# Kernel optimization log

Hardware: AMD Instinct MI355X
Metric: run time of the kernel (lower is better)

The kernel has to match this reference:

```python
import jax, jax.numpy as jnp
import numpy as np

E = 64        # num_local_experts
N = 32768     # total permuted tokens
H = 1024      # hidden_dim
F = 1024      # intermediate_dim
C = N // E    # per-expert capacity (setup uses equal token counts)


def setup_inputs() -> dict:
    key = jax.random.key(0)
    k1, k2, k3, k4 = jax.random.split(key, 4)
    s = 0.02  # init scale
    return {
        "permuted_local_hidden_states": jax.random.normal(k1, (N, H), jnp.float32),
        "tokens_per_expert": jnp.full((E,), C, dtype=jnp.int32),
        "w_gate": jax.random.normal(k2, (E, H, F), jnp.float32) * s,
        "w_up": jax.random.normal(k3, (E, H, F), jnp.float32) * s,
        "w_down": jax.random.normal(k4, (E, F, H), jnp.float32) * s,
    }


def reference(permuted_local_hidden_states, tokens_per_expert, w_gate, w_up, w_down):
    x = permuted_local_hidden_states  # [N, H], sorted by expert
    counts = tokens_per_expert.astype(jnp.int32)  # [E]
    # start offset of each expert's contiguous token range (torch cumsum + cat([0]))
    starts = jnp.concatenate([jnp.zeros((1,), jnp.int32), jnp.cumsum(counts)])[:-1]
    # expert id and within-expert position for every token (jit-friendly dispatch)
    eid = jnp.repeat(jnp.arange(E, dtype=jnp.int32), counts, total_repeat_length=N)
    pos = jnp.arange(N, dtype=jnp.int32) - starts[eid]
    # gather tokens into fixed-capacity per-expert buffer [E, C, H]; unused slots stay 0
    buf = jnp.zeros((E, C, H), x.dtype).at[eid, pos].set(x)
    # grouped LLaMA MLP: down( silu(gate(x)) * up(x) ), one GEMM triple per expert, batched
    gate = jnp.einsum('ech,ehf->ecf', buf, w_gate)
    up = jnp.einsum('ech,ehf->ecf', buf, w_up)
    h = jax.nn.silu(gate) * up                      # [E, C, F]
    out_buf = jnp.einsum('ecf,efh->ech', h, w_down)  # [E, C, H]
    # scatter back to flat token order (output_local[start:end] = output)
    output_local = out_buf[eid, pos]  # [N, H]
    return output_local
```

## Files before the change

kernel.cpp:

```cpp
#include <hip/hip_runtime.h>
#include <stdint.h>


#define NUM_E 64
#define DIM_H 1024
#define DIM_F 1024
#define CAP   512
#define NTOK  32768

typedef short short8 __attribute__((ext_vector_type(8)));
typedef float f32x4 __attribute__((ext_vector_type(4)));

#define VMCNT(n)  asm volatile("s_waitcnt vmcnt(" #n ")" ::: "memory")
#define LGKMCNT0  asm volatile("s_waitcnt lgkmcnt(0)" ::: "memory")
#define SBAR      __builtin_amdgcn_s_barrier()
#define SCHED0    __builtin_amdgcn_sched_barrier(0)

__device__ __forceinline__ uint32_t cvtpk(float lo, float hi) {
  uint32_t r;
  asm("v_cvt_pk_bf16_f32 %0, %1, %2" : "=v"(r) : "v"(lo), "v"(hi));
  return r;
}
__device__ __forceinline__ unsigned short f2bf(float a) {
  uint32_t ua = __builtin_bit_cast(uint32_t, a);
  ua += 0x7FFFu + ((ua >> 16) & 1u);
  return (unsigned short)(ua >> 16);
}
__device__ __forceinline__ void gload_lds16(const void* g, void* l) {
  __builtin_amdgcn_global_load_lds((const __attribute__((address_space(1))) uint32_t*)g,
                                   (__attribute__((address_space(3))) uint32_t*)l, 16, 0, 0);
}

__global__ __launch_bounds__(256) void cvt_kernel(const float* __restrict__ x,
                                                  unsigned short* __restrict__ xbf) {
  size_t i = ((size_t)blockIdx.x * 256 + threadIdx.x) * 8;
  f32x4 a = *reinterpret_cast<const f32x4*>(x + i);
  f32x4 b = *reinterpret_cast<const f32x4*>(x + i + 4);
  int4 o = make_int4((int)cvtpk(a[0], a[1]), (int)cvtpk(a[2], a[3]),
                     (int)cvtpk(b[0], b[1]), (int)cvtpk(b[2], b[3]));
  *reinterpret_cast<int4*>(xbf + i) = o;
}

__global__ __launch_bounds__(512, 2) void gateup_kernel_v3(
    const unsigned short* __restrict__ xbf, const float* __restrict__ wg,
    const float* __restrict__ wu, unsigned short* __restrict__ hout)
{
  __shared__ unsigned char smem[131072];
  const int t = threadIdx.x;
  int bid = blockIdx.x;
  bid = (bid & 7) * 128 + (bid >> 3);
  const int e = bid >> 4, rr = bid & 15, mb = rr >> 3, nb = rr & 7;
  const int row0 = e * CAP + mb * 256;
  const int col0 = nb * 128;
  const unsigned short* Ag = xbf + (size_t)row0 * DIM_H;
  const float* Bgg = wg + (size_t)e * (DIM_H * DIM_F) + col0;
  const float* Bug = wu + (size_t)e * (DIM_H * DIM_F) + col0;

  const int lane = t & 63, wid = t >> 6;
  const int wm = wid >> 1, wn = wid & 1;

  f32x4 accg[4][4], accu[4][4];
  #pragma unroll
  for (int i = 0; i < 4; i++)
    #pragma unroll
    for (int j = 0; j < 4; j++) {
      accg[i][j] = f32x4{0.f, 0.f, 0.f, 0.f};
      accu[i][j] = f32x4{0.f, 0.f, 0.f, 0.f};
    }

  const int bn = t & 127, bkb = (t >> 7) * 16;
  float bg[16], bu[16];

  auto loadB = [&](int k0) {
    #pragma unroll
    for (int i = 0; i < 16; i++) {
      bg[i] = Bgg[(size_t)(k0 + bkb + i) * DIM_F + bn];
      bu[i] = Bug[(size_t)(k0 + bkb + i) * DIM_F + bn];
    }
  };
  auto writeB = [&](int b) {
    const int Bb = 65536 + b * 32768;
    #pragma unroll
    for (int j = 0; j < 4; j++) {
      int off = Bb + bn * 128 + (((bkb + j * 4) * 2) ^ ((bn & 7) << 4));
      *reinterpret_cast<uint2*>(&smem[off]) =
          make_uint2(cvtpk(bg[j*4+0], bg[j*4+1]), cvtpk(bg[j*4+2], bg[j*4+3]));
      *reinterpret_cast<uint2*>(&smem[off + 16384]) =
          make_uint2(cvtpk(bu[j*4+0], bu[j*4+1]), cvtpk(bu[j*4+2], bu[j*4+3]));
    }
  };
  auto loadA = [&](int k0, int buf) {
    #pragma unroll
    for (int j = 0; j < 4; j++) {
      int lin = (j * 512 + t) * 16;
      int r = lin >> 7;
      int q = (lin >> 4) & 7;
      const void* src = (const unsigned char*)Ag + (size_t)r * 2048 + k0 * 2 + ((q ^ (r & 7)) * 16);
      gload_lds16(src, &smem[buf * 32768 + lin]);
    }
  };
  auto compute = [&](int kt) {
    const int Ab = (kt & 1) * 32768;
    const int Bb = 65536 + (kt & 1) * 32768;
    __builtin_amdgcn_s_setprio(1);
    #pragma unroll
    for (int kk = 0; kk < 2; kk++) {
      short8 a[4], bgf[4], buf_[4];
      #pragma unroll
      for (int mi = 0; mi < 4; mi++) {
        int r = wm * 64 + mi * 16 + (lane & 15);
        a[mi] = *reinterpret_cast<const short8*>(
            &smem[Ab + r * 128 + ((kk * 64 + (lane >> 4) * 16) ^ ((r & 7) << 4))]);
      }
      #pragma unroll
      for (int ni = 0; ni < 4; ni++) {
        int n = wn * 64 + ni * 16 + (lane & 15);
        int off = Bb + n * 128 + ((kk * 64 + (lane >> 4) * 16) ^ ((n & 7) << 4));
        bgf[ni]  = *reinterpret_cast<const short8*>(&smem[off]);
        buf_[ni] = *reinterpret_cast<const short8*>(&smem[off + 16384]);
      }
      #pragma unroll
      for (int mi = 0; mi < 4; mi++)
        #pragma unroll
        for (int ni = 0; ni < 4; ni++) {
          accg[mi][ni] = __builtin_amdgcn_mfma_f32_16x16x32_bf16(a[mi], bgf[ni],  accg[mi][ni], 0, 0, 0);
          accu[mi][ni] = __builtin_amdgcn_mfma_f32_16x16x32_bf16(a[mi], buf_[ni], accu[mi][ni], 0, 0, 0);
        }
    }
    __builtin_amdgcn_s_setprio(0);
  };

  const int NT = DIM_H / 64;
  loadB(0);
  loadA(0, 0);
  VMCNT(4); SCHED0;
  writeB(0);
  LGKMCNT0; VMCNT(0); SCHED0;
  SBAR;
  for (int kt = 0; kt < NT; kt++) {
    if (kt + 1 < NT) {
      loadB((kt + 1) * 64);
      loadA((kt + 1) * 64, (kt + 1) & 1);
      SCHED0;
    }
    compute(kt);
    if (kt + 1 < NT) {
      VMCNT(4); SCHED0;
      writeB((kt + 1) & 1);
      LGKMCNT0; VMCNT(0); SCHED0;
      SBAR;
    }
  }

  #pragma unroll
  for (int mi = 0; mi < 4; mi++)
    #pragma unroll
    for (int ni = 0; ni < 4; ni++) {
      int col = col0 + wn * 64 + ni * 16 + (lane & 15);
      int rbase = row0 + wm * 64 + mi * 16 + (lane >> 4) * 4;
      #pragma unroll
      for (int j = 0; j < 4; j++) {
        float g = accg[mi][ni][j], u = accu[mi][ni][j];
        float hv = (g / (1.f + __expf(-g))) * u;
        hout[(size_t)(rbase + j) * DIM_F + col] = f2bf(hv);
      }
    }
}

__global__ __launch_bounds__(512, 2) void down_kernel_v3(
    const unsigned short* __restrict__ hin, const float* __restrict__ wd,
    float* __restrict__ out)
{
  __shared__ unsigned char smem[98304];
  const int t = threadIdx.x;
  int bid = blockIdx.x;
  bid = (bid & 7) * 128 + (bid >> 3);
  const int e = bid >> 4, rr = bid & 15, mb = rr >> 3, nb = rr & 7;
  const int row0 = e * CAP + mb * 256;
  const int col0 = nb * 128;
  const unsigned short* Ag = hin + (size_t)row0 * DIM_F;
  const float* Bdg = wd + (size_t)e * (DIM_F * DIM_H) + col0;

  const int lane = t & 63, wid = t >> 6;
  const int wm = wid >> 1, wn = wid & 1;

  f32x4 acc[4][4];
  #pragma unroll
  for (int i = 0; i < 4; i++)
    #pragma unroll
    for (int j = 0; j < 4; j++) acc[i][j] = f32x4{0.f, 0.f, 0.f, 0.f};

  const int bn = t & 127, bkb = (t >> 7) * 16;
  float bs[16];

  auto loadB = [&](int k0) {
    #pragma unroll
    for (int i = 0; i < 16; i++)
      bs[i] = Bdg[(size_t)(k0 + bkb + i) * DIM_H + bn];
  };
  auto writeB = [&](int b) {
    const int Bb = 65536 + b * 16384;
    #pragma unroll
    for (int j = 0; j < 4; j++) {
      int off = Bb + bn * 128 + (((bkb + j * 4) * 2) ^ ((bn & 7) << 4));
      *reinterpret_cast<uint2*>(&smem[off]) =
          make_uint2(cvtpk(bs[j*4+0], bs[j*4+1]), cvtpk(bs[j*4+2], bs[j*4+3]));
    }
  };
  auto loadA = [&](int k0, int buf) {
    #pragma unroll
    for (int j = 0; j < 4; j++) {
      int lin = (j * 512 + t) * 16;
      int r = lin >> 7;
      int q = (lin >> 4) & 7;
      const void* src = (const unsigned char*)Ag + (size_t)r * 2048 + k0 * 2 + ((q ^ (r & 7)) * 16);
      gload_lds16(src, &smem[buf * 32768 + lin]);
    }
  };
  auto compute = [&](int kt) {
    const int Ab = (kt & 1) * 32768;
    const int Bb = 65536 + (kt & 1) * 16384;
    __builtin_amdgcn_s_setprio(1);
    #pragma unroll
    for (int kk = 0; kk < 2; kk++) {
      short8 a[4], b[4];
      #pragma unroll
      for (int mi = 0; mi < 4; mi++) {
        int r = wm * 64 + mi * 16 + (lane & 15);
        a[mi] = *reinterpret_cast<const short8*>(
            &smem[Ab + r * 128 + ((kk * 64 + (lane >> 4) * 16) ^ ((r & 7) << 4))]);
      }
      #pragma unroll
      for (int ni = 0; ni < 4; ni++) {
        int n = wn * 64 + ni * 16 + (lane & 15);
        b[ni] = *reinterpret_cast<const short8*>(
            &smem[Bb + n * 128 + ((kk * 64 + (lane >> 4) * 16) ^ ((n & 7) << 4))]);
      }
      #pragma unroll
      for (int mi = 0; mi < 4; mi++)
        #pragma unroll
        for (int ni = 0; ni < 4; ni++)
          acc[mi][ni] = __builtin_amdgcn_mfma_f32_16x16x32_bf16(a[mi], b[ni], acc[mi][ni], 0, 0, 0);
    }
    __builtin_amdgcn_s_setprio(0);
  };

  const int NT = DIM_F / 64;
  loadB(0);
  loadA(0, 0);
  VMCNT(4); SCHED0;
  writeB(0);
  LGKMCNT0; VMCNT(0); SCHED0;
  SBAR;
  for (int kt = 0; kt < NT; kt++) {
    if (kt + 1 < NT) {
      loadB((kt + 1) * 64);
      loadA((kt + 1) * 64, (kt + 1) & 1);
      SCHED0;
    }
    compute(kt);
    if (kt + 1 < NT) {
      VMCNT(4); SCHED0;
      writeB((kt + 1) & 1);
      LGKMCNT0; VMCNT(0); SCHED0;
      SBAR;
    }
  }

  #pragma unroll
  for (int mi = 0; mi < 4; mi++)
    #pragma unroll
    for (int ni = 0; ni < 4; ni++) {
      int col = col0 + wn * 64 + ni * 16 + (lane & 15);
      int rbase = row0 + wm * 64 + mi * 16 + (lane >> 4) * 4;
      #pragma unroll
      for (int j = 0; j < 4; j++)
        out[(size_t)(rbase + j) * DIM_H + col] = acc[mi][ni][j];
    }
}

extern "C" void kernel_launch(void* const* d_in, const int* in_sizes, int n_in,
                              void* d_out, int out_size, void* d_ws, size_t ws_size,
                              hipStream_t stream) {
  (void)in_sizes; (void)n_in; (void)out_size; (void)ws_size;
  const float* x  = (const float*)d_in[0];
  const float* wg = (const float*)d_in[2];
  const float* wu = (const float*)d_in[3];
  const float* wd = (const float*)d_in[4];
  unsigned short* h   = (unsigned short*)d_ws;
  unsigned short* xbf = (unsigned short*)((char*)d_ws + (size_t)NTOK * DIM_F * 2);
  float* out = (float*)d_out;

  cvt_kernel<<<dim3((NTOK * DIM_H) / (256 * 8)), dim3(256), 0, stream>>>(x, xbf);
  gateup_kernel_v3<<<dim3(1024), dim3(512), 0, stream>>>(xbf, wg, wu, h);
  down_kernel_v3<<<dim3(1024), dim3(512), 0, stream>>>(h, wd, out);
}
```

Baseline: 365.2 us.

## Triple-buffer A tiles in LDS to prefetch two k-steps ahead

Both GEMM kernels now keep three LDS buffers for the A tile and issue the direct-to-LDS A load two iterations ahead instead of one. The waits move to vmcnt(4), so the newest A loads stay in flight across the barrier. This is meant to hide global-load latency for the activation operand behind compute. The cost is more LDS (160KB for gate/up, 128KB for down) and slightly more complex wait logic at the loop tail.

```diff
diff --git a/kernel.cpp b/kernel.cpp
--- a/kernel.cpp
+++ b/kernel.cpp
@@ -41,11 +41,11 @@
   *reinterpret_cast<int4*>(xbf + i) = o;
 }
 
-__global__ __launch_bounds__(512, 2) void gateup_kernel_v3(
+__global__ __launch_bounds__(512, 2) void gateup_kernel_v9(
     const unsigned short* __restrict__ xbf, const float* __restrict__ wg,
     const float* __restrict__ wu, unsigned short* __restrict__ hout)
 {
-  __shared__ unsigned char smem[131072];
+  __shared__ unsigned char smem[163840];
   const int t = threadIdx.x;
   int bid = blockIdx.x;
   bid = (bid & 7) * 128 + (bid >> 3);
@@ -79,7 +79,7 @@
     }
   };
   auto writeB = [&](int b) {
-    const int Bb = 65536 + b * 32768;
+    const int Bb = 98304 + b * 32768;
     #pragma unroll
     for (int j = 0; j < 4; j++) {
       int off = Bb + bn * 128 + (((bkb + j * 4) * 2) ^ ((bn & 7) << 4));
@@ -100,8 +100,8 @@
     }
   };
   auto compute = [&](int kt) {
-    const int Ab = (kt & 1) * 32768;
-    const int Bb = 65536 + (kt & 1) * 32768;
+    const int Ab = (kt % 3) * 32768;
+    const int Bb = 98304 + (kt & 1) * 32768;
     __builtin_amdgcn_s_setprio(1);
     #pragma unroll
     for (int kk = 0; kk < 2; kk++) {
@@ -133,21 +133,25 @@
   const int NT = DIM_H / 64;
   loadB(0);
   loadA(0, 0);
+  SCHED0;
   VMCNT(4); SCHED0;
   writeB(0);
-  LGKMCNT0; VMCNT(0); SCHED0;
+  loadA(64, 1);
+  SCHED0;
+  LGKMCNT0; VMCNT(4); SCHED0;
   SBAR;
   for (int kt = 0; kt < NT; kt++) {
     if (kt + 1 < NT) {
       loadB((kt + 1) * 64);
-      loadA((kt + 1) * 64, (kt + 1) & 1);
+      if (kt + 2 < NT) loadA((kt + 2) * 64, (kt + 2) % 3);
       SCHED0;
     }
     compute(kt);
     if (kt + 1 < NT) {
-      VMCNT(4); SCHED0;
+      if (kt + 2 < NT) { VMCNT(4); } else { VMCNT(0); }
+      SCHED0;
       writeB((kt + 1) & 1);
-      LGKMCNT0; VMCNT(0); SCHED0;
+      LGKMCNT0; SCHED0;
       SBAR;
     }
   }
@@ -160,18 +164,18 @@
       int rbase = row0 + wm * 64 + mi * 16 + (lane >> 4) * 4;
       #pragma unroll
       for (int j = 0; j < 4; j++) {
-        float g = accg[mi][ni][j], u = accu[mi][ni][j];
-        float hv = (g / (1.f + __expf(-g))) * u;
+        float gv = accg[mi][ni][j], uv = accu[mi][ni][j];
+        float hv = (gv / (1.f + __expf(-gv))) * uv;
         hout[(size_t)(rbase + j) * DIM_F + col] = f2bf(hv);
       }
     }
 }
 
-__global__ __launch_bounds__(512, 2) void down_kernel_v3(
+__global__ __launch_bounds__(512, 2) void down_kernel_v9(
     const unsigned short* __restrict__ hin, const float* __restrict__ wd,
     float* __restrict__ out)
 {
-  __shared__ unsigned char smem[98304];
+  __shared__ unsigned char smem[131072];
   const int t = threadIdx.x;
   int bid = blockIdx.x;
   bid = (bid & 7) * 128 + (bid >> 3);
@@ -199,7 +203,7 @@
       bs[i] = Bdg[(size_t)(k0 + bkb + i) * DIM_H + bn];
   };
   auto writeB = [&](int b) {
-    const int Bb = 65536 + b * 16384;
+    const int Bb = 98304 + b * 16384;
     #pragma unroll
     for (int j = 0; j < 4; j++) {
       int off = Bb + bn * 128 + (((bkb + j * 4) * 2) ^ ((bn & 7) << 4));
@@ -218,8 +222,8 @@
     }
   };
   auto compute = [&](int kt) {
-    const int Ab = (kt & 1) * 32768;
-    const int Bb = 65536 + (kt & 1) * 16384;
+    const int Ab = (kt % 3) * 32768;
+    const int Bb = 98304 + (kt & 1) * 16384;
     __builtin_amdgcn_s_setprio(1);
     #pragma unroll
     for (int kk = 0; kk < 2; kk++) {
@@ -248,21 +252,25 @@
   const int NT = DIM_F / 64;
   loadB(0);
   loadA(0, 0);
+  SCHED0;
   VMCNT(4); SCHED0;
   writeB(0);
-  LGKMCNT0; VMCNT(0); SCHED0;
+  loadA(64, 1);
+  SCHED0;
+  LGKMCNT0; VMCNT(4); SCHED0;
   SBAR;
   for (int kt = 0; kt < NT; kt++) {
     if (kt + 1 < NT) {
       loadB((kt + 1) * 64);
-      loadA((kt + 1) * 64, (kt + 1) & 1);
+      if (kt + 2 < NT) loadA((kt + 2) * 64, (kt + 2) % 3);
       SCHED0;
     }
     compute(kt);
     if (kt + 1 < NT) {
-      VMCNT(4); SCHED0;
+      if (kt + 2 < NT) { VMCNT(4); } else { VMCNT(0); }
+      SCHED0;
       writeB((kt + 1) & 1);
-      LGKMCNT0; VMCNT(0); SCHED0;
+      LGKMCNT0; SCHED0;
       SBAR;
     }
   }
@@ -292,6 +300,6 @@
   float* out = (float*)d_out;
 
   cvt_kernel<<<dim3((NTOK * DIM_H) / (256 * 8)), dim3(256), 0, stream>>>(x, xbf);
-  gateup_kernel_v3<<<dim3(1024), dim3(512), 0, stream>>>(xbf, wg, wu, h);
-  down_kernel_v3<<<dim3(1024), dim3(512), 0, stream>>>(h, wd, out);
-}
+  gateup_kernel_v9<<<dim3(1024), dim3(512), 0, stream>>>(xbf, wg, wu, h);
+  down_kernel_v9<<<dim3(1024), dim3(512), 0, stream>>>(h, wd, out);
+}
```

Result: no change. 369.5 us (+1.2%).

## Interleave LDS reads, global prefetch and MFMA clusters in four-phase K loop

Applied to the files above, without the earlier changes.

Both GEMM kernels restructure the per-K-tile loop into four barrier-separated phases. Each phase issues LDS fragment reads and a slice of the next tile's global loads (A, B first half, B second half, then the B write to LDS), followed by a prioritized MFMA cluster. The goal is to spread memory traffic across the compute phases and keep the matrix units fed, instead of one bulk load and write per tile. In exchange it adds many extra workgroup barriers per tile and uses #pragma unroll 1, which may add synchronization overhead.

```diff
diff --git a/kernel.cpp b/kernel.cpp
--- a/kernel.cpp
+++ b/kernel.cpp
@@ -15,6 +15,8 @@
 #define LGKMCNT0  asm volatile("s_waitcnt lgkmcnt(0)" ::: "memory")
 #define SBAR      __builtin_amdgcn_s_barrier()
 #define SCHED0    __builtin_amdgcn_sched_barrier(0)
+#define SP1       __builtin_amdgcn_s_setprio(1)
+#define SP0       __builtin_amdgcn_s_setprio(0)
 
 __device__ __forceinline__ uint32_t cvtpk(float lo, float hi) {
   uint32_t r;
@@ -41,7 +43,7 @@
   *reinterpret_cast<int4*>(xbf + i) = o;
 }
 
-__global__ __launch_bounds__(512, 2) void gateup_kernel_v3(
+__global__ __launch_bounds__(512, 2) void gateup_kernel_v11(
     const unsigned short* __restrict__ xbf, const float* __restrict__ wg,
     const float* __restrict__ wu, unsigned short* __restrict__ hout)
 {
@@ -71,9 +73,16 @@
   const int bn = t & 127, bkb = (t >> 7) * 16;
   float bg[16], bu[16];
 
-  auto loadB = [&](int k0) {
-    #pragma unroll
-    for (int i = 0; i < 16; i++) {
+  auto loadB1 = [&](int k0) {
+    #pragma unroll
+    for (int i = 0; i < 8; i++) {
+      bg[i] = Bgg[(size_t)(k0 + bkb + i) * DIM_F + bn];
+      bu[i] = Bug[(size_t)(k0 + bkb + i) * DIM_F + bn];
+    }
+  };
+  auto loadB2 = [&](int k0) {
+    #pragma unroll
+    for (int i = 8; i < 16; i++) {
       bg[i] = Bgg[(size_t)(k0 + bkb + i) * DIM_F + bn];
       bu[i] = Bug[(size_t)(k0 + bkb + i) * DIM_F + bn];
     }
@@ -99,57 +108,78 @@
       gload_lds16(src, &smem[buf * 32768 + lin]);
     }
   };
-  auto compute = [&](int kt) {
+  auto ldA = [&](short8 (&a)[4], int Ab, int kk) {
+    #pragma unroll
+    for (int mi = 0; mi < 4; mi++) {
+      int r = wm * 64 + mi * 16 + (lane & 15);
+      a[mi] = *reinterpret_cast<const short8*>(
+          &smem[Ab + r * 128 + ((kk * 64 + (lane >> 4) * 16) ^ ((r & 7) << 4))]);
+    }
+  };
+  auto ldB = [&](short8 (&bf)[4], int Bb, int kk, int uoff) {
+    #pragma unroll
+    for (int ni = 0; ni < 4; ni++) {
+      int n = wn * 64 + ni * 16 + (lane & 15);
+      bf[ni] = *reinterpret_cast<const short8*>(
+          &smem[Bb + uoff + n * 128 + ((kk * 64 + (lane >> 4) * 16) ^ ((n & 7) << 4))]);
+    }
+  };
+  auto mfq = [&](f32x4 (&acc)[4][4], const short8 (&a)[4], const short8 (&bf)[4]) {
+    SP1;
+    #pragma unroll
+    for (int mi = 0; mi < 4; mi++)
+      #pragma unroll
+      for (int ni = 0; ni < 4; ni++)
+        acc[mi][ni] = __builtin_amdgcn_mfma_f32_16x16x32_bf16(a[mi], bf[ni], acc[mi][ni], 0, 0, 0);
+    SP0;
+  };
+
+  const int NT = DIM_H / 64;
+  loadB1(0); loadB2(0);
+  loadA(0, 0);
+  SCHED0;
+  VMCNT(4); SCHED0;
+  writeB(0);
+  VMCNT(0); LGKMCNT0; SCHED0;
+  SBAR;
+
+  #pragma unroll 1
+  for (int kt = 0; kt < NT; kt++) {
     const int Ab = (kt & 1) * 32768;
     const int Bb = 65536 + (kt & 1) * 32768;
-    __builtin_amdgcn_s_setprio(1);
-    #pragma unroll
-    for (int kk = 0; kk < 2; kk++) {
-      short8 a[4], bgf[4], buf_[4];
-      #pragma unroll
-      for (int mi = 0; mi < 4; mi++) {
-        int r = wm * 64 + mi * 16 + (lane & 15);
-        a[mi] = *reinterpret_cast<const short8*>(
-            &smem[Ab + r * 128 + ((kk * 64 + (lane >> 4) * 16) ^ ((r & 7) << 4))]);
-      }
-      #pragma unroll
-      for (int ni = 0; ni < 4; ni++) {
-        int n = wn * 64 + ni * 16 + (lane & 15);
-        int off = Bb + n * 128 + ((kk * 64 + (lane >> 4) * 16) ^ ((n & 7) << 4));
-        bgf[ni]  = *reinterpret_cast<const short8*>(&smem[off]);
-        buf_[ni] = *reinterpret_cast<const short8*>(&smem[off + 16384]);
-      }
-      #pragma unroll
-      for (int mi = 0; mi < 4; mi++)
-        #pragma unroll
-        for (int ni = 0; ni < 4; ni++) {
-          accg[mi][ni] = __builtin_amdgcn_mfma_f32_16x16x32_bf16(a[mi], bgf[ni],  accg[mi][ni], 0, 0, 0);
-          accu[mi][ni] = __builtin_amdgcn_mfma_f32_16x16x32_bf16(a[mi], buf_[ni], accu[mi][ni], 0, 0, 0);
-        }
-    }
-    __builtin_amdgcn_s_setprio(0);
-  };
-
-  const int NT = DIM_H / 64;
-  loadB(0);
-  loadA(0, 0);
-  VMCNT(4); SCHED0;
-  writeB(0);
-  LGKMCNT0; VMCNT(0); SCHED0;
-  SBAR;
-  for (int kt = 0; kt < NT; kt++) {
-    if (kt + 1 < NT) {
-      loadB((kt + 1) * 64);
-      loadA((kt + 1) * 64, (kt + 1) & 1);
-      SCHED0;
-    }
-    compute(kt);
-    if (kt + 1 < NT) {
-      VMCNT(4); SCHED0;
+    const bool more = (kt + 1 < NT);
+    short8 a[4], bf[4];
+    ldA(a, Ab, 0); ldB(bf, Bb, 0, 0);
+    if (more) loadA((kt + 1) * 64, (kt + 1) & 1);
+    SCHED0;
+    SBAR;
+    LGKMCNT0; SCHED0;
+    mfq(accg, a, bf);
+    SBAR;
+    ldB(bf, Bb, 0, 16384);
+    if (more) loadB1((kt + 1) * 64);
+    SCHED0;
+    SBAR;
+    LGKMCNT0; SCHED0;
+    mfq(accu, a, bf);
+    SBAR;
+    ldA(a, Ab, 1); ldB(bf, Bb, 1, 0);
+    if (more) loadB2((kt + 1) * 64);
+    SCHED0;
+    SBAR;
+    LGKMCNT0; SCHED0;
+    mfq(accg, a, bf);
+    SBAR;
+    ldB(bf, Bb, 1, 16384);
+    if (more) {
+      VMCNT(0); SCHED0;
       writeB((kt + 1) & 1);
-      LGKMCNT0; VMCNT(0); SCHED0;
-      SBAR;
-    }
+    }
+    SCHED0;
+    SBAR;
+    LGKMCNT0; SCHED0;
+    mfq(accu, a, bf);
+    SBAR;
   }
 
   #pragma unroll
@@ -160,14 +190,14 @@
       int rbase = row0 + wm * 64 + mi * 16 + (lane >> 4) * 4;
       #pragma unroll
       for (int j = 0; j < 4; j++) {
-        float g = accg[mi][ni][j], u = accu[mi][ni][j];
-        float hv = (g / (1.f + __expf(-g))) * u;
+        float gv = accg[mi][ni][j], uv = accu[mi][ni][j];
+        float hv = (gv / (1.f + __expf(-gv))) * uv;
         hout[(size_t)(rbase + j) * DIM_F + col] = f2bf(hv);
       }
     }
 }
 
-__global__ __launch_bounds__(512, 2) void down_kernel_v3(
+__global__ __launch_bounds__(512, 2) void down_kernel_v11(
     const unsigned short* __restrict__ hin, const float* __restrict__ wd,
     float* __restrict__ out)
 {
@@ -193,9 +223,14 @@
   const int bn = t & 127, bkb = (t >> 7) * 16;
   float bs[16];
 
-  auto loadB = [&](int k0) {
-    #pragma unroll
-    for (int i = 0; i < 16; i++)
+  auto loadB1 = [&](int k0) {
+    #pragma unroll
+    for (int i = 0; i < 8; i++)
+      bs[i] = Bdg[(size_t)(k0 + bkb + i) * DIM_H + bn];
+  };
+  auto loadB2 = [&](int k0) {
+    #pragma unroll
+    for (int i = 8; i < 16; i++)
       bs[i] = Bdg[(size_t)(k0 + bkb + i) * DIM_H + bn];
   };
   auto writeB = [&](int b) {
@@ -217,54 +252,79 @@
       gload_lds16(src, &smem[buf * 32768 + lin]);
     }
   };
-  auto compute = [&](int kt) {
+  auto ldA = [&](short8 (&a)[4], int Ab, int kk) {
+    #pragma unroll
+    for (int mi = 0; mi < 4; mi++) {
+      int r = wm * 64 + mi * 16 + (lane & 15);
+      a[mi] = *reinterpret_cast<const short8*>(
+          &smem[Ab + r * 128 + ((kk * 64 + (lane >> 4) * 16) ^ ((r & 7) << 4))]);
+    }
+  };
+  auto ldB2f = [&](short8 (&bf)[2], int Bb, int kk, int nh) {
+    #pragma unroll
+    for (int i = 0; i < 2; i++) {
+      int n = wn * 64 + (nh * 2 + i) * 16 + (lane & 15);
+      bf[i] = *reinterpret_cast<const short8*>(
+          &smem[Bb + n * 128 + ((kk * 64 + (lane >> 4) * 16) ^ ((n & 7) << 4))]);
+    }
+  };
+  auto mf8 = [&](const short8 (&a)[4], const short8 (&bf)[2], int nh) {
+    SP1;
+    #pragma unroll
+    for (int mi = 0; mi < 4; mi++)
+      #pragma unroll
+      for (int i = 0; i < 2; i++)
+        acc[mi][nh * 2 + i] =
+            __builtin_amdgcn_mfma_f32_16x16x32_bf16(a[mi], bf[i], acc[mi][nh * 2 + i], 0, 0, 0);
+    SP0;
+  };
+
+  const int NT = DIM_F / 64;
+  loadB1(0); loadB2(0);
+  loadA(0, 0);
+  SCHED0;
+  VMCNT(4); SCHED0;
+  writeB(0);
+  VMCNT(0); LGKMCNT0; SCHED0;
+  SBAR;
+
+  #pragma unroll 1
+  for (int kt = 0; kt < NT; kt++) {
     const int Ab = (kt & 1) * 32768;
     const int Bb = 65536 + (kt & 1) * 16384;
-    __builtin_amdgcn_s_setprio(1);
-    #pragma unroll
-    for (int kk = 0; kk < 2; kk++) {
-      short8 a[4], b[4];
-      #pragma unroll
-      for (int mi = 0; mi < 4; mi++) {
-        int r = wm * 64 + mi * 16 + (lane & 15);
-        a[mi] = *reinterpret_cast<const short8*>(
-            &smem[Ab + r * 128 + ((kk * 64 + (lane >> 4) * 16) ^ ((r & 7) << 4))]);
-      }
-      #pragma unroll
-      for (int ni = 0; ni < 4; ni++) {
-        int n = wn * 64 + ni * 16 + (lane & 15);
-        b[ni] = *reinterpret_cast<const short8*>(
-            &smem[Bb + n * 128 + ((kk * 64 + (lane >> 4) * 16) ^ ((n & 7) << 4))]);
-      }
-      #pragma unroll
-      for (int mi = 0; mi < 4; mi++)
-        #pragma unroll
-        for (int ni = 0; ni < 4; ni++)
-          acc[mi][ni] = __builtin_amdgcn_mfma_f32_16x16x32_bf16(a[mi], b[ni], acc[mi][ni], 0, 0, 0);
-    }
-    __builtin_amdgcn_s_setprio(0);
-  };
-
-  const int NT = DIM_F / 64;
-  loadB(0);
-  loadA(0, 0);
-  VMCNT(4); SCHED0;
-  writeB(0);
-  LGKMCNT0; VMCNT(0); SCHED0;
-  SBAR;
-  for (int kt = 0; kt < NT; kt++) {
-    if (kt + 1 < NT) {
-      loadB((kt + 1) * 64);
-      loadA((kt + 1) * 64, (kt + 1) & 1);
-      SCHED0;
-    }
-    compute(kt);
-    if (kt + 1 < NT) {
-      VMCNT(4); SCHED0;
+    const bool more = (kt + 1 < NT);
+    short8 a[4], bf[2];
+    ldA(a, Ab, 0); ldB2f(bf, Bb, 0, 0);
+    if (more) loadA((kt + 1) * 64, (kt + 1) & 1);
+    SCHED0;
+    SBAR;
+    LGKMCNT0; SCHED0;
+    mf8(a, bf, 0);
+    SBAR;
+    ldB2f(bf, Bb, 0, 1);
+    if (more) loadB1((kt + 1) * 64);
+    SCHED0;
+    SBAR;
+    LGKMCNT0; SCHED0;
+    mf8(a, bf, 1);
+    SBAR;
+    ldA(a, Ab, 1); ldB2f(bf, Bb, 1, 0);
+    if (more) loadB2((kt + 1) * 64);
+    SCHED0;
+    SBAR;
+    LGKMCNT0; SCHED0;
+    mf8(a, bf, 0);
+    SBAR;
+    ldB2f(bf, Bb, 1, 1);
+    if (more) {
+      VMCNT(0); SCHED0;
       writeB((kt + 1) & 1);
-      LGKMCNT0; VMCNT(0); SCHED0;
-      SBAR;
-    }
+    }
+    SCHED0;
+    SBAR;
+    LGKMCNT0; SCHED0;
+    mf8(a, bf, 1);
+    SBAR;
   }
 
   #pragma unroll
@@ -292,6 +352,6 @@
   float* out = (float*)d_out;
 
   cvt_kernel<<<dim3((NTOK * DIM_H) / (256 * 8)), dim3(256), 0, stream>>>(x, xbf);
-  gateup_kernel_v3<<<dim3(1024), dim3(512), 0, stream>>>(xbf, wg, wu, h);
-  down_kernel_v3<<<dim3(1024), dim3(512), 0, stream>>>(h, wd, out);
-}
+  gateup_kernel_v11<<<dim3(1024), dim3(512), 0, stream>>>(xbf, wg, wu, h);
+  down_kernel_v11<<<dim3(1024), dim3(512), 0, stream>>>(h, wd, out);
+}
```

Result: slower. 442.7 us (+21.2%).

## Halve N tile to 64 and single-buffer B in LDS for higher occupancy

Applied to the files above, without the earlier changes.

Both GEMM kernels shrink the output tile from 256x128 to 256x64, doubling the grid to 2048 blocks and halving the accumulator registers. B in LDS goes from double-buffered to single-buffered, guarded by an extra barrier before each write, and each thread now writes B with one 16-byte store per matrix. LDS per block drops to 80KB and 72KB, and launch bounds now request four waves per SIMD, aiming to hide latency through more resident work. The cost is that each A tile is reloaded by twice as many blocks, arithmetic intensity per block falls, and the extra barrier per k-step can stall the pipeline.

```diff
diff --git a/kernel.cpp b/kernel.cpp
--- a/kernel.cpp
+++ b/kernel.cpp
@@ -41,17 +41,17 @@
   *reinterpret_cast<int4*>(xbf + i) = o;
 }
 
-__global__ __launch_bounds__(512, 2) void gateup_kernel_v3(
+__global__ __launch_bounds__(512, 4) void gateup_kernel_v12(
     const unsigned short* __restrict__ xbf, const float* __restrict__ wg,
     const float* __restrict__ wu, unsigned short* __restrict__ hout)
 {
-  __shared__ unsigned char smem[131072];
+  __shared__ unsigned char smem[81920];
   const int t = threadIdx.x;
   int bid = blockIdx.x;
-  bid = (bid & 7) * 128 + (bid >> 3);
-  const int e = bid >> 4, rr = bid & 15, mb = rr >> 3, nb = rr & 7;
+  bid = (bid & 7) * 256 + (bid >> 3);
+  const int e = bid >> 5, rr = bid & 31, mb = rr >> 4, nb = rr & 15;
   const int row0 = e * CAP + mb * 256;
-  const int col0 = nb * 128;
+  const int col0 = nb * 64;
   const unsigned short* Ag = xbf + (size_t)row0 * DIM_H;
   const float* Bgg = wg + (size_t)e * (DIM_H * DIM_F) + col0;
   const float* Bug = wu + (size_t)e * (DIM_H * DIM_F) + col0;
@@ -59,35 +59,33 @@
   const int lane = t & 63, wid = t >> 6;
   const int wm = wid >> 1, wn = wid & 1;
 
-  f32x4 accg[4][4], accu[4][4];
+  f32x4 accg[4][2], accu[4][2];
   #pragma unroll
   for (int i = 0; i < 4; i++)
     #pragma unroll
-    for (int j = 0; j < 4; j++) {
+    for (int j = 0; j < 2; j++) {
       accg[i][j] = f32x4{0.f, 0.f, 0.f, 0.f};
       accu[i][j] = f32x4{0.f, 0.f, 0.f, 0.f};
     }
 
-  const int bn = t & 127, bkb = (t >> 7) * 16;
-  float bg[16], bu[16];
+  const int bn = t & 63, bkb = (t >> 6) * 8;
+  float bg[8], bu[8];
 
   auto loadB = [&](int k0) {
     #pragma unroll
-    for (int i = 0; i < 16; i++) {
+    for (int i = 0; i < 8; i++) {
       bg[i] = Bgg[(size_t)(k0 + bkb + i) * DIM_F + bn];
       bu[i] = Bug[(size_t)(k0 + bkb + i) * DIM_F + bn];
     }
   };
-  auto writeB = [&](int b) {
-    const int Bb = 65536 + b * 32768;
-    #pragma unroll
-    for (int j = 0; j < 4; j++) {
-      int off = Bb + bn * 128 + (((bkb + j * 4) * 2) ^ ((bn & 7) << 4));
-      *reinterpret_cast<uint2*>(&smem[off]) =
-          make_uint2(cvtpk(bg[j*4+0], bg[j*4+1]), cvtpk(bg[j*4+2], bg[j*4+3]));
-      *reinterpret_cast<uint2*>(&smem[off + 16384]) =
-          make_uint2(cvtpk(bu[j*4+0], bu[j*4+1]), cvtpk(bu[j*4+2], bu[j*4+3]));
-    }
+  auto writeB = [&]() {
+    int off = 65536 + bn * 128 + ((bkb * 2) ^ ((bn & 7) << 4));
+    *reinterpret_cast<int4*>(&smem[off]) =
+        make_int4((int)cvtpk(bg[0], bg[1]), (int)cvtpk(bg[2], bg[3]),
+                  (int)cvtpk(bg[4], bg[5]), (int)cvtpk(bg[6], bg[7]));
+    *reinterpret_cast<int4*>(&smem[off + 8192]) =
+        make_int4((int)cvtpk(bu[0], bu[1]), (int)cvtpk(bu[2], bu[3]),
+                  (int)cvtpk(bu[4], bu[5]), (int)cvtpk(bu[6], bu[7]));
   };
   auto loadA = [&](int k0, int buf) {
     #pragma unroll
@@ -101,11 +99,10 @@
   };
   auto compute = [&](int kt) {
     const int Ab = (kt & 1) * 32768;
-    const int Bb = 65536 + (kt & 1) * 32768;
     __builtin_amdgcn_s_setprio(1);
     #pragma unroll
     for (int kk = 0; kk < 2; kk++) {
-      short8 a[4], bgf[4], buf_[4];
+      short8 a[4], bgf[2], buf_[2];
       #pragma unroll
       for (int mi = 0; mi < 4; mi++) {
         int r = wm * 64 + mi * 16 + (lane & 15);
@@ -113,16 +110,16 @@
             &smem[Ab + r * 128 + ((kk * 64 + (lane >> 4) * 16) ^ ((r & 7) << 4))]);
       }
       #pragma unroll
-      for (int ni = 0; ni < 4; ni++) {
-        int n = wn * 64 + ni * 16 + (lane & 15);
-        int off = Bb + n * 128 + ((kk * 64 + (lane >> 4) * 16) ^ ((n & 7) << 4));
+      for (int ni = 0; ni < 2; ni++) {
+        int n = wn * 32 + ni * 16 + (lane & 15);
+        int off = 65536 + n * 128 + ((kk * 64 + (lane >> 4) * 16) ^ ((n & 7) << 4));
         bgf[ni]  = *reinterpret_cast<const short8*>(&smem[off]);
-        buf_[ni] = *reinterpret_cast<const short8*>(&smem[off + 16384]);
+        buf_[ni] = *reinterpret_cast<const short8*>(&smem[off + 8192]);
       }
       #pragma unroll
       for (int mi = 0; mi < 4; mi++)
         #pragma unroll
-        for (int ni = 0; ni < 4; ni++) {
+        for (int ni = 0; ni < 2; ni++) {
           accg[mi][ni] = __builtin_amdgcn_mfma_f32_16x16x32_bf16(a[mi], bgf[ni],  accg[mi][ni], 0, 0, 0);
           accu[mi][ni] = __builtin_amdgcn_mfma_f32_16x16x32_bf16(a[mi], buf_[ni], accu[mi][ni], 0, 0, 0);
         }
@@ -133,21 +130,25 @@
   const int NT = DIM_H / 64;
   loadB(0);
   loadA(0, 0);
+  SCHED0;
   VMCNT(4); SCHED0;
-  writeB(0);
-  LGKMCNT0; VMCNT(0); SCHED0;
+  writeB();
+  VMCNT(0); LGKMCNT0; SCHED0;
   SBAR;
+  #pragma unroll 1
   for (int kt = 0; kt < NT; kt++) {
-    if (kt + 1 < NT) {
+    const bool more = (kt + 1 < NT);
+    if (more) {
       loadB((kt + 1) * 64);
       loadA((kt + 1) * 64, (kt + 1) & 1);
       SCHED0;
     }
     compute(kt);
-    if (kt + 1 < NT) {
+    if (more) {
+      SBAR;
       VMCNT(4); SCHED0;
-      writeB((kt + 1) & 1);
-      LGKMCNT0; VMCNT(0); SCHED0;
+      writeB();
+      VMCNT(0); LGKMCNT0; SCHED0;
       SBAR;
     }
   }
@@ -155,57 +156,54 @@
   #pragma unroll
   for (int mi = 0; mi < 4; mi++)
     #pragma unroll
-    for (int ni = 0; ni < 4; ni++) {
-      int col = col0 + wn * 64 + ni * 16 + (lane & 15);
+    for (int ni = 0; ni < 2; ni++) {
+      int col = col0 + wn * 32 + ni * 16 + (lane & 15);
       int rbase = row0 + wm * 64 + mi * 16 + (lane >> 4) * 4;
       #pragma unroll
       for (int j = 0; j < 4; j++) {
-        float g = accg[mi][ni][j], u = accu[mi][ni][j];
-        float hv = (g / (1.f + __expf(-g))) * u;
+        float gv = accg[mi][ni][j], uv = accu[mi][ni][j];
+        float hv = (gv / (1.f + __expf(-gv))) * uv;
         hout[(size_t)(rbase + j) * DIM_F + col] = f2bf(hv);
       }
     }
 }
 
-__global__ __launch_bounds__(512, 2) void down_kernel_v3(
+__global__ __launch_bounds__(512, 4) void down_kernel_v12(
     const unsigned short* __restrict__ hin, const float* __restrict__ wd,
     float* __restrict__ out)
 {
-  __shared__ unsigned char smem[98304];
+  __shared__ unsigned char smem[73728];
   const int t = threadIdx.x;
   int bid = blockIdx.x;
-  bid = (bid & 7) * 128 + (bid >> 3);
-  const int e = bid >> 4, rr = bid & 15, mb = rr >> 3, nb = rr & 7;
+  bid = (bid & 7) * 256 + (bid >> 3);
+  const int e = bid >> 5, rr = bid & 31, mb = rr >> 4, nb = rr & 15;
   const int row0 = e * CAP + mb * 256;
-  const int col0 = nb * 128;
+  const int col0 = nb * 64;
   const unsigned short* Ag = hin + (size_t)row0 * DIM_F;
   const float* Bdg = wd + (size_t)e * (DIM_F * DIM_H) + col0;
 
   const int lane = t & 63, wid = t >> 6;
   const int wm = wid >> 1, wn = wid & 1;
 
-  f32x4 acc[4][4];
+  f32x4 acc[4][2];
   #pragma unroll
   for (int i = 0; i < 4; i++)
     #pragma unroll
-    for (int j = 0; j < 4; j++) acc[i][j] = f32x4{0.f, 0.f, 0.f, 0.f};
-
-  const int bn = t & 127, bkb = (t >> 7) * 16;
-  float bs[16];
+    for (int j = 0; j < 2; j++) acc[i][j] = f32x4{0.f, 0.f, 0.f, 0.f};
+
+  const int bn = t & 63, bkb = (t >> 6) * 8;
+  float bs[8];
 
   auto loadB = [&](int k0) {
     #pragma unroll
-    for (int i = 0; i < 16; i++)
+    for (int i = 0; i < 8; i++)
       bs[i] = Bdg[(size_t)(k0 + bkb + i) * DIM_H + bn];
   };
-  auto writeB = [&](int b) {
-    const int Bb = 65536 + b * 16384;
-    #pragma unroll
-    for (int j = 0; j < 4; j++) {
-      int off = Bb + bn * 128 + (((bkb + j * 4) * 2) ^ ((bn & 7) << 4));
-      *reinterpret_cast<uint2*>(&smem[off]) =
-          make_uint2(cvtpk(bs[j*4+0], bs[j*4+1]), cvtpk(bs[j*4+2], bs[j*4+3]));
-    }
+  auto writeB = [&]() {
+    int off = 65536 + bn * 128 + ((bkb * 2) ^ ((bn & 7) << 4));
+    *reinterpret_cast<int4*>(&smem[off]) =
+        make_int4((int)cvtpk(bs[0], bs[1]), (int)cvtpk(bs[2], bs[3]),
+                  (int)cvtpk(bs[4], bs[5]), (int)cvtpk(bs[6], bs[7]));
   };
   auto loadA = [&](int k0, int buf) {
     #pragma unroll
@@ -219,11 +217,10 @@
   };
   auto compute = [&](int kt) {
     const int Ab = (kt & 1) * 32768;
-    const int Bb = 65536 + (kt & 1) * 16384;
     __builtin_amdgcn_s_setprio(1);
     #pragma unroll
     for (int kk = 0; kk < 2; kk++) {
-      short8 a[4], b[4];
+      short8 a[4], b[2];
       #pragma unroll
       for (int mi = 0; mi < 4; mi++) {
         int r = wm * 64 + mi * 16 + (lane & 15);
@@ -231,15 +228,15 @@
             &smem[Ab + r * 128 + ((kk * 64 + (lane >> 4) * 16) ^ ((r & 7) << 4))]);
       }
       #pragma unroll
-      for (int ni = 0; ni < 4; ni++) {
-        int n = wn * 64 + ni * 16 + (lane & 15);
+      for (int ni = 0; ni < 2; ni++) {
+        int n = wn * 32 + ni * 16 + (lane & 15);
         b[ni] = *reinterpret_cast<const short8*>(
-            &smem[Bb + n * 128 + ((kk * 64 + (lane >> 4) * 16) ^ ((n & 7) << 4))]);
+            &smem[65536 + n * 128 + ((kk * 64 + (lane >> 4) * 16) ^ ((n & 7) << 4))]);
       }
       #pragma unroll
       for (int mi = 0; mi < 4; mi++)
         #pragma unroll
-        for (int ni = 0; ni < 4; ni++)
+        for (int ni = 0; ni < 2; ni++)
           acc[mi][ni] = __builtin_amdgcn_mfma_f32_16x16x32_bf16(a[mi], b[ni], acc[mi][ni], 0, 0, 0);
     }
     __builtin_amdgcn_s_setprio(0);
@@ -248,21 +245,25 @@
   const int NT = DIM_F / 64;
   loadB(0);
   loadA(0, 0);
+  SCHED0;
   VMCNT(4); SCHED0;
-  writeB(0);
-  LGKMCNT0; VMCNT(0); SCHED0;
+  writeB();
+  VMCNT(0); LGKMCNT0; SCHED0;
   SBAR;
+  #pragma unroll 1
   for (int kt = 0; kt < NT; kt++) {
-    if (kt + 1 < NT) {
+    const bool more = (kt + 1 < NT);
+    if (more) {
       loadB((kt + 1) * 64);
       loadA((kt + 1) * 64, (kt + 1) & 1);
       SCHED0;
     }
     compute(kt);
-    if (kt + 1 < NT) {
+    if (more) {
+      SBAR;
       VMCNT(4); SCHED0;
-      writeB((kt + 1) & 1);
-      LGKMCNT0; VMCNT(0); SCHED0;
+      writeB();
+      VMCNT(0); LGKMCNT0; SCHED0;
       SBAR;
     }
   }
@@ -270,8 +271,8 @@
   #pragma unroll
   for (int mi = 0; mi < 4; mi++)
     #pragma unroll
-    for (int ni = 0; ni < 4; ni++) {
-      int col = col0 + wn * 64 + ni * 16 + (lane & 15);
+    for (int ni = 0; ni < 2; ni++) {
+      int col = col0 + wn * 32 + ni * 16 + (lane & 15);
       int rbase = row0 + wm * 64 + mi * 16 + (lane >> 4) * 4;
       #pragma unroll
       for (int j = 0; j < 4; j++)
@@ -292,6 +293,6 @@
   float* out = (float*)d_out;
 
   cvt_kernel<<<dim3((NTOK * DIM_H) / (256 * 8)), dim3(256), 0, stream>>>(x, xbf);
-  gateup_kernel_v3<<<dim3(1024), dim3(512), 0, stream>>>(xbf, wg, wu, h);
-  down_kernel_v3<<<dim3(1024), dim3(512), 0, stream>>>(h, wd, out);
-}
+  gateup_kernel_v12<<<dim3(2048), dim3(512), 0, stream>>>(xbf, wg, wu, h);
+  down_kernel_v12<<<dim3(2048), dim3(512), 0, stream>>>(h, wd, out);
+}
```

Result: slower. 374.7 us (+2.6%).
